# Kernel optimization log

Measured on AMD Instinct MI355X. Metric: run time of the kernel, lower is better.

The kernel has to match this reference:

```python
import jax, jax.numpy as jnp
import numpy as np

T, B, E, H = 2048, 4, 1024, 16
D = E // H  # head_dim = 64


def setup_inputs() -> dict:
    key = jax.random.key(0)
    k1, k2, k3, k4 = jax.random.split(key, 4)
    x = jax.random.normal(k1, (T, B, E), dtype=jnp.float32)
    # xavier-ish init scale
    Wqkv = jax.random.normal(k2, (3 * E, E), dtype=jnp.float32) * (1.0 / np.sqrt(2.0 * E))
    Wo = jax.random.normal(k3, (E, E), dtype=jnp.float32) * (1.0 / np.sqrt(E))
    key_padding_mask = jax.random.randint(k4, (B, T), 0, 2).astype(jnp.bool_)  # True = pad
    return {"x": x, "Wqkv": Wqkv, "Wo": Wo, "key_padding_mask": key_padding_mask}


def reference(x, Wqkv, Wo, key_padding_mask):
    t, b, e = x.shape
    h, d = H, E // H
    # fused QKV projection (bias=False)
    qkv = jnp.einsum('tbe,fe->tbf', x, Wqkv).reshape(t, b, 3, h, d)
    # chunk along the 3-axis, then permute to (B, H, T, D)
    q = jnp.transpose(qkv[:, :, 0], (1, 2, 0, 3))
    k = jnp.transpose(qkv[:, :, 1], (1, 2, 0, 3))
    v = jnp.transpose(qkv[:, :, 2], (1, 2, 0, 3))
    # SDPA with default scale 1/sqrt(head_dim); additive -inf mask on padded keys
    scale = 1.0 / jnp.sqrt(jnp.asarray(d, dtype=x.dtype))
    scores = jnp.einsum('bhtd,bhsd->bhts', q, k) * scale
    scores = jnp.where(key_padding_mask[:, None, None, :], -jnp.inf, scores)
    probs = jax.nn.softmax(scores, axis=-1)
    ctx = jnp.einsum('bhts,bhsd->bhtd', probs, v)  # (B,H,T,D)
    ctx = jnp.transpose(ctx, (0, 2, 1, 3)).reshape(b, t, e)  # (B,T,E)
    out = jnp.einsum('bte,fe->btf', ctx, Wo)  # out_proj, bias=False
    return jnp.transpose(out, (1, 0, 2))  # back to (T,B,E)
```

## Files before the change

kernel.cpp:

```cpp
#include <hip/hip_runtime.h>

typedef unsigned short u16;
typedef __bf16 bf16x8 __attribute__((ext_vector_type(8)));
typedef unsigned short u16x8 __attribute__((ext_vector_type(8)));
typedef unsigned short u16x4 __attribute__((ext_vector_type(4)));
typedef float f32x4 __attribute__((ext_vector_type(4)));

__device__ __forceinline__ f32x4 mfma16(u16x8 a, u16x8 b, f32x4 c) {
    return __builtin_amdgcn_mfma_f32_16x16x32_bf16(
        __builtin_bit_cast(bf16x8, a), __builtin_bit_cast(bf16x8, b), c, 0, 0, 0);
}

__device__ __forceinline__ u16 f2b(float f) {
    unsigned int u = __builtin_bit_cast(unsigned int, f);
    return (u16)((u + 0x7fffu + ((u >> 16) & 1u)) >> 16);
}

__device__ __forceinline__ f32x4 zero4() { f32x4 z = {0.f, 0.f, 0.f, 0.f}; return z; }

typedef __attribute__((address_space(1))) const unsigned int gas_u32;
typedef __attribute__((address_space(3))) unsigned int las_u32;
__device__ __forceinline__ void gload16(const u16* g, u16* l) {
    __builtin_amdgcn_global_load_lds((gas_u32*)g, (las_u32*)l, 16, 0, 0);
}

__device__ __forceinline__ u16x4 tr16(unsigned off) {
    u16x4 r;
    asm volatile("ds_read_b64_tr_b16 %0, %1" : "=v"(r) : "v"(off));
    return r;
}

__global__ __launch_bounds__(256) void cvt_bf16_kernel(const float* __restrict__ in,
                                                       u16* __restrict__ out, int n) {
    int i = (blockIdx.x * 256 + threadIdx.x) * 4;
    if (i >= n) return;
    float4 v = *reinterpret_cast<const float4*>(in + i);
    u16x4 o;
    o.x = f2b(v.x); o.y = f2b(v.y); o.z = f2b(v.z); o.w = f2b(v.w);
    *reinterpret_cast<u16x4*>(out + i) = o;
}

__global__ void detect_mask_kernel(const unsigned char* __restrict__ m, int* __restrict__ flag) {
    __shared__ int any;
    if (threadIdx.x == 0) any = 0;
    __syncthreads();
    int acc = 0;
    for (int i = threadIdx.x; i < 8192; i += 256)
        if (i & 3) acc |= m[i];
    if (acc) atomicOr(&any, 1);
    __syncthreads();
    if (threadIdx.x == 0) *flag = any ? 0 : 1;
}

template <int EPI>
__global__ __launch_bounds__(256)
void gemm_bt_kernel(const u16* __restrict__ A, const u16* __restrict__ Bt,
                    int M, int N, int K,
                    u16* __restrict__ qo, u16* __restrict__ ko, u16* __restrict__ vo,
                    float* __restrict__ fo) {
    constexpr int BK = 64;
    __shared__ __align__(16) u16 Al[128 * BK];
    __shared__ __align__(16) u16 Bl[128 * BK];
    int tid = threadIdx.x;
    int wave = tid >> 6, lane = tid & 63;
    int l15 = lane & 15, l16 = lane >> 4;
    int wr = wave >> 1, wc = wave & 1;
    int bx = blockIdx.x, by = blockIdx.y;

    const u16* gA[4]; const u16* gB[4]; u16* lA[4]; u16* lB[4];
#pragma unroll
    for (int q = 0; q < 4; q++) {
        int c = tid + q * 256;
        gA[q] = A + (size_t)(by * 128 + (c >> 3)) * K + (c & 7) * 8;
        gB[q] = Bt + (size_t)(bx * 128 + (c >> 3)) * K + (c & 7) * 8;
        lA[q] = Al + c * 8;
        lB[q] = Bl + c * 8;
    }

    f32x4 acc[4][4];
#pragma unroll
    for (int m = 0; m < 4; m++)
#pragma unroll
        for (int n = 0; n < 4; n++) acc[m][n] = zero4();

    for (int k0 = 0; k0 < K; k0 += BK) {
        __syncthreads();
#pragma unroll
        for (int q = 0; q < 4; q++) {
            gload16(gA[q] + k0, lA[q]);
            gload16(gB[q] + k0, lB[q]);
        }
        __syncthreads();
#pragma unroll
        for (int ks = 0; ks < 2; ks++) {
            u16x8 af[4], bfr[4];
#pragma unroll
            for (int m = 0; m < 4; m++)
                af[m] = *(const u16x8*)&Al[(wr * 64 + m * 16 + l15) * BK + ks * 32 + l16 * 8];
#pragma unroll
            for (int n = 0; n < 4; n++)
                bfr[n] = *(const u16x8*)&Bl[(wc * 64 + n * 16 + l15) * BK + ks * 32 + l16 * 8];
#pragma unroll
            for (int m = 0; m < 4; m++)
#pragma unroll
                for (int n = 0; n < 4; n++) acc[m][n] = mfma16(af[m], bfr[n], acc[m][n]);
        }
    }

#pragma unroll
    for (int m = 0; m < 4; m++) {
#pragma unroll
        for (int j = 0; j < 4; j++) {
            int row = by * 128 + wr * 64 + m * 16 + l16 * 4 + j;
#pragma unroll
            for (int n = 0; n < 4; n++) {
                int col = bx * 128 + wc * 64 + n * 16 + l15;
                float val = acc[m][n][j];
                if constexpr (EPI == 0) {
                    int chunk = col >> 10, h = (col >> 6) & 15, d = col & 63;
                    int t = row >> 2, bI = row & 3;
                    if (chunk == 0) val *= 0.18033688011112042f;
                    u16* dst = (chunk == 0) ? qo : (chunk == 1) ? ko : vo;
                    dst[((size_t)(bI * 16 + h) * 2048 + t) * 64 + d] = f2b(val);
                } else {
                    fo[(size_t)row * N + col] = val;
                }
            }
        }
    }
}

__global__ __launch_bounds__(256)
void attn_kernel(const u16* __restrict__ Qg, const u16* __restrict__ Kg,
                 const u16* __restrict__ Vg, const void* __restrict__ maskp,
                 const int* __restrict__ flag, u16* __restrict__ ctx) {
    __shared__ __align__(16) u16 Kl[32 * 72];
    __shared__ __align__(128) u16 Vs[2048];
    __shared__ __align__(16) u16 Pl[4][32 * 40];

    int tid = threadIdx.x;
    int wave = tid >> 6, lane = tid & 63;
    int l15 = lane & 15, l16 = lane >> 4;
    int bh = blockIdx.y;
    int b = bh >> 4, h = bh & 15;
    size_t base = (size_t)bh * 2048 * 64;
    int q0 = blockIdx.x * 128 + wave * 32;

    int isInt = *flag;
    const unsigned char* m8 = (const unsigned char*)maskp;
    const int* m32 = (const int*)maskp;

    u16x8 aq[2][2];
#pragma unroll
    for (int qb = 0; qb < 2; qb++)
#pragma unroll
        for (int ks = 0; ks < 2; ks++)
            aq[qb][ks] = *(const u16x8*)(Qg + base + (size_t)(q0 + qb * 16 + l15) * 64 +
                                         ks * 32 + l16 * 8);

    f32x4 acc_o[2][4];
    float mrun[2][4], plsum[2][4];
#pragma unroll
    for (int qb = 0; qb < 2; qb++) {
#pragma unroll
        for (int db = 0; db < 4; db++) acc_o[qb][db] = zero4();
#pragma unroll
        for (int j = 0; j < 4; j++) { mrun[qb][j] = -1e30f; plsum[qb][j] = 0.f; }
    }

    int srow = tid >> 3, schunk = tid & 7;
    const u16* kg = Kg + base + (size_t)srow * 64 + schunk * 8;
    const u16* vg = Vg + base + (size_t)srow * 64 + schunk * 8;
    u16* kldst = &Kl[srow * 72 + schunk * 8];
    u16* vsdst = &Vs[(schunk >> 1) * 512 + srow * 16 + (schunk & 1) * 8];
    unsigned vtrb = (unsigned)(uintptr_t)(&Vs[0]) + (unsigned)(l16 * 256 + l15 * 8);

    u16x8 kv = *(const u16x8*)kg;
    u16x8 vv = *(const u16x8*)vg;

    for (int it = 0; it < 64; ++it) {
        int s0 = it * 32;
        __syncthreads();
        *(u16x8*)kldst = kv;
        *(u16x8*)vsdst = vv;
        int snext = (s0 + 32) & 2047;
        u16x8 kv2 = *(const u16x8*)(kg + (size_t)snext * 64);
        u16x8 vv2 = *(const u16x8*)(vg + (size_t)snext * 64);
        __syncthreads();

        int ki = b * 2048 + s0 + l15;
        int pad0 = isInt ? (m32[ki] != 0) : (m8[ki] != 0);
        int pad1 = isInt ? (m32[ki + 16] != 0) : (m8[ki + 16] != 0);

        f32x4 sa[2][2];
        sa[0][0] = zero4(); sa[0][1] = zero4(); sa[1][0] = zero4(); sa[1][1] = zero4();
#pragma unroll
        for (int kb = 0; kb < 2; kb++)
#pragma unroll
            for (int ks = 0; ks < 2; ks++) {
                u16x8 bk = *(const u16x8*)&Kl[(kb * 16 + l15) * 72 + ks * 32 + l16 * 8];
                sa[0][kb] = mfma16(aq[0][ks], bk, sa[0][kb]);
                sa[1][kb] = mfma16(aq[1][ks], bk, sa[1][kb]);
            }

#pragma unroll
        for (int qb = 0; qb < 2; qb++) {
            float s0v[4], s1v[4];
            float gl = -1e30f;
#pragma unroll
            for (int j = 0; j < 4; j++) {
                s0v[j] = pad0 ? -1e30f : sa[qb][0][j];
                s1v[j] = pad1 ? -1e30f : sa[qb][1][j];
                gl = fmaxf(gl, fmaxf(s0v[j], s1v[j]) - mrun[qb][j]);
            }
            if (__any(gl > 8.0f)) {
                float tm[4];
#pragma unroll
                for (int j = 0; j < 4; j++) tm[j] = fmaxf(s0v[j], s1v[j]);
#pragma unroll
                for (int j = 0; j < 4; j++) {
                    tm[j] = fmaxf(tm[j], __shfl_xor(tm[j], 1));
                    tm[j] = fmaxf(tm[j], __shfl_xor(tm[j], 2));
                    tm[j] = fmaxf(tm[j], __shfl_xor(tm[j], 4));
                    tm[j] = fmaxf(tm[j], __shfl_xor(tm[j], 8));
                }
#pragma unroll
                for (int j = 0; j < 4; j++) {
                    float mnew = fmaxf(mrun[qb][j], tm[j]);
                    float sc = exp2f(mrun[qb][j] - mnew);
                    mrun[qb][j] = mnew;
                    plsum[qb][j] *= sc;
#pragma unroll
                    for (int db = 0; db < 4; db++) acc_o[qb][db][j] *= sc;
                }
            }
#pragma unroll
            for (int j = 0; j < 4; j++) {
                float p0 = exp2f(s0v[j] - mrun[qb][j]);
                float p1 = exp2f(s1v[j] - mrun[qb][j]);
                int prow = qb * 16 + l16 * 4 + j;
                Pl[wave][prow * 40 + l15] = f2b(p0);
                Pl[wave][prow * 40 + 16 + l15] = f2b(p1);
                plsum[qb][j] += p0 + p1;
            }
        }

        u16x8 ap0 = *(const u16x8*)&Pl[wave][(0 * 16 + l15) * 40 + l16 * 8];
        u16x8 ap1 = *(const u16x8*)&Pl[wave][(1 * 16 + l15) * 40 + l16 * 8];
#pragma unroll
        for (int db = 0; db < 4; db++) {
            u16x4 t0 = tr16(vtrb + db * 1024);
            u16x4 t1 = tr16(vtrb + db * 1024 + 128);
            asm volatile("s_waitcnt lgkmcnt(0)" ::: "memory");
            __builtin_amdgcn_sched_barrier(0);
            u16x8 bv = {t0[0], t0[1], t0[2], t0[3], t1[0], t1[1], t1[2], t1[3]};
            acc_o[0][db] = mfma16(ap0, bv, acc_o[0][db]);
            acc_o[1][db] = mfma16(ap1, bv, acc_o[1][db]);
        }
        kv = kv2; vv = vv2;
    }

#pragma unroll
    for (int qb = 0; qb < 2; qb++)
#pragma unroll
        for (int j = 0; j < 4; j++) {
            float rs = plsum[qb][j];
            rs += __shfl_xor(rs, 1);
            rs += __shfl_xor(rs, 2);
            rs += __shfl_xor(rs, 4);
            rs += __shfl_xor(rs, 8);
            float inv = 1.0f / rs;
            int qg = q0 + qb * 16 + l16 * 4 + j;
            size_t mrow = (size_t)qg * 4 + b;
#pragma unroll
            for (int db = 0; db < 4; db++)
                ctx[mrow * 1024 + h * 64 + db * 16 + l15] = f2b(acc_o[qb][db][j] * inv);
        }
}

extern "C" void kernel_launch(void* const* d_in, const int* in_sizes, int n_in,
                              void* d_out, int out_size, void* d_ws, size_t ws_size,
                              hipStream_t stream) {
    const float* x = (const float*)d_in[0];
    const float* wqkv = (const float*)d_in[1];
    const float* wo = (const float*)d_in[2];
    const void* mask = d_in[3];
    float* out = (float*)d_out;

    char* ws = (char*)d_ws;
    int* flag = (int*)ws;
    u16* xb = (u16*)(ws + 16);
    u16* wqkvb = xb + 8388608;
    u16* wob = wqkvb + 3145728;
    u16* qw = wob + 1048576;
    u16* kw = qw + 8388608;
    u16* vw = kw + 8388608;
    u16* ctx = xb;

    cvt_bf16_kernel<<<8192, 256, 0, stream>>>(x, xb, 8388608);
    cvt_bf16_kernel<<<3072, 256, 0, stream>>>(wqkv, wqkvb, 3145728);
    cvt_bf16_kernel<<<1024, 256, 0, stream>>>(wo, wob, 1048576);
    detect_mask_kernel<<<1, 256, 0, stream>>>((const unsigned char*)mask, flag);

    gemm_bt_kernel<0><<<dim3(24, 64), 256, 0, stream>>>(xb, wqkvb, 8192, 3072, 1024,
                                                        qw, kw, vw, nullptr);
    attn_kernel<<<dim3(16, 64), 256, 0, stream>>>(qw, kw, vw, mask, flag, ctx);
    gemm_bt_kernel<1><<<dim3(8, 64), 256, 0, stream>>>(ctx, wob, 8192, 1024, 1024,
                                                       nullptr, nullptr, nullptr, out);
}
```

Measured before the change: 451.9 us.

## Double attention key tile to 64 and batch V transposed loads before MFMAs

```diff
diff --git a/kernel.cpp b/kernel.cpp
--- a/kernel.cpp
+++ b/kernel.cpp
@@ -130,13 +130,13 @@
     }
 }
 
-__global__ __launch_bounds__(256)
+__global__ __launch_bounds__(256, 3)
 void attn_kernel(const u16* __restrict__ Qg, const u16* __restrict__ Kg,
                  const u16* __restrict__ Vg, const void* __restrict__ maskp,
                  const int* __restrict__ flag, u16* __restrict__ ctx) {
-    __shared__ __align__(16) u16 Kl[32 * 72];
-    __shared__ __align__(128) u16 Vs[2048];
-    __shared__ __align__(16) u16 Pl[4][32 * 40];
+    __shared__ __align__(16) u16 Kl[64 * 72];
+    __shared__ __align__(128) u16 Vs[4][64][16];
+    __shared__ __align__(16) u16 Pl[4][32 * 72];
 
     int tid = threadIdx.x;
     int wave = tid >> 6, lane = tid & 63;
@@ -168,55 +168,65 @@
         for (int j = 0; j < 4; j++) { mrun[qb][j] = -1e30f; plsum[qb][j] = 0.f; }
     }
 
-    int srow = tid >> 3, schunk = tid & 7;
-    const u16* kg = Kg + base + (size_t)srow * 64 + schunk * 8;
-    const u16* vg = Vg + base + (size_t)srow * 64 + schunk * 8;
-    u16* kldst = &Kl[srow * 72 + schunk * 8];
-    u16* vsdst = &Vs[(schunk >> 1) * 512 + srow * 16 + (schunk & 1) * 8];
-    unsigned vtrb = (unsigned)(uintptr_t)(&Vs[0]) + (unsigned)(l16 * 256 + l15 * 8);
-
-    u16x8 kv = *(const u16x8*)kg;
-    u16x8 vv = *(const u16x8*)vg;
-
-    for (int it = 0; it < 64; ++it) {
-        int s0 = it * 32;
+    int srow2 = tid >> 2, sc2 = tid & 3;
+    const u16* kg2 = Kg + base + (size_t)srow2 * 64 + sc2 * 16;
+    const u16* vg2 = Vg + base + (size_t)srow2 * 64 + sc2 * 16;
+    u16* kld = &Kl[srow2 * 72 + sc2 * 16];
+    u16* vsd = &Vs[sc2][srow2][0];
+    unsigned vtrb = (unsigned)(uintptr_t)(&Vs[0][0][0]) + (unsigned)(l16 * 256 + l15 * 8);
+
+    u16x8 ka = *(const u16x8*)kg2, kb_ = *(const u16x8*)(kg2 + 8);
+    u16x8 va = *(const u16x8*)vg2, vb_ = *(const u16x8*)(vg2 + 8);
+
+    for (int it = 0; it < 32; ++it) {
+        int s0 = it * 64;
         __syncthreads();
-        *(u16x8*)kldst = kv;
-        *(u16x8*)vsdst = vv;
-        int snext = (s0 + 32) & 2047;
-        u16x8 kv2 = *(const u16x8*)(kg + (size_t)snext * 64);
-        u16x8 vv2 = *(const u16x8*)(vg + (size_t)snext * 64);
+        *(u16x8*)kld = ka; *(u16x8*)(kld + 8) = kb_;
+        *(u16x8*)vsd = va; *(u16x8*)(vsd + 8) = vb_;
+        int snext = (s0 + 64) & 2047;
+        u16x8 kan = *(const u16x8*)(kg2 + (size_t)snext * 64);
+        u16x8 kbn = *(const u16x8*)(kg2 + (size_t)snext * 64 + 8);
+        u16x8 van = *(const u16x8*)(vg2 + (size_t)snext * 64);
+        u16x8 vbn = *(const u16x8*)(vg2 + (size_t)snext * 64 + 8);
         __syncthreads();
 
-        int ki = b * 2048 + s0 + l15;
-        int pad0 = isInt ? (m32[ki] != 0) : (m8[ki] != 0);
-        int pad1 = isInt ? (m32[ki + 16] != 0) : (m8[ki + 16] != 0);
-
-        f32x4 sa[2][2];
-        sa[0][0] = zero4(); sa[0][1] = zero4(); sa[1][0] = zero4(); sa[1][1] = zero4();
-#pragma unroll
-        for (int kb = 0; kb < 2; kb++)
+        int pad[4];
+#pragma unroll
+        for (int kb2 = 0; kb2 < 4; kb2++) {
+            int ki = b * 2048 + s0 + kb2 * 16 + l15;
+            pad[kb2] = isInt ? (m32[ki] != 0) : (m8[ki] != 0);
+        }
+
+        f32x4 sa[2][4];
+#pragma unroll
+        for (int kb2 = 0; kb2 < 4; kb2++) { sa[0][kb2] = zero4(); sa[1][kb2] = zero4(); }
+        __builtin_amdgcn_s_setprio(1);
+#pragma unroll
+        for (int kb2 = 0; kb2 < 4; kb2++)
 #pragma unroll
             for (int ks = 0; ks < 2; ks++) {
-                u16x8 bk = *(const u16x8*)&Kl[(kb * 16 + l15) * 72 + ks * 32 + l16 * 8];
-                sa[0][kb] = mfma16(aq[0][ks], bk, sa[0][kb]);
-                sa[1][kb] = mfma16(aq[1][ks], bk, sa[1][kb]);
-            }
+                u16x8 bk = *(const u16x8*)&Kl[(kb2 * 16 + l15) * 72 + ks * 32 + l16 * 8];
+                sa[0][kb2] = mfma16(aq[0][ks], bk, sa[0][kb2]);
+                sa[1][kb2] = mfma16(aq[1][ks], bk, sa[1][kb2]);
+            }
+        __builtin_amdgcn_s_setprio(0);
 
 #pragma unroll
         for (int qb = 0; qb < 2; qb++) {
-            float s0v[4], s1v[4];
+            float sv[4][4];
             float gl = -1e30f;
 #pragma unroll
-            for (int j = 0; j < 4; j++) {
-                s0v[j] = pad0 ? -1e30f : sa[qb][0][j];
-                s1v[j] = pad1 ? -1e30f : sa[qb][1][j];
-                gl = fmaxf(gl, fmaxf(s0v[j], s1v[j]) - mrun[qb][j]);
-            }
+            for (int kb2 = 0; kb2 < 4; kb2++)
+#pragma unroll
+                for (int j = 0; j < 4; j++) {
+                    sv[kb2][j] = pad[kb2] ? -1e30f : sa[qb][kb2][j];
+                    gl = fmaxf(gl, sv[kb2][j] - mrun[qb][j]);
+                }
             if (__any(gl > 8.0f)) {
                 float tm[4];
 #pragma unroll
-                for (int j = 0; j < 4; j++) tm[j] = fmaxf(s0v[j], s1v[j]);
+                for (int j = 0; j < 4; j++)
+                    tm[j] = fmaxf(fmaxf(sv[0][j], sv[1][j]), fmaxf(sv[2][j], sv[3][j]));
 #pragma unroll
                 for (int j = 0; j < 4; j++) {
                     tm[j] = fmaxf(tm[j], __shfl_xor(tm[j], 1));
@@ -236,28 +246,48 @@
             }
 #pragma unroll
             for (int j = 0; j < 4; j++) {
-                float p0 = exp2f(s0v[j] - mrun[qb][j]);
-                float p1 = exp2f(s1v[j] - mrun[qb][j]);
                 int prow = qb * 16 + l16 * 4 + j;
-                Pl[wave][prow * 40 + l15] = f2b(p0);
-                Pl[wave][prow * 40 + 16 + l15] = f2b(p1);
-                plsum[qb][j] += p0 + p1;
-            }
-        }
-
-        u16x8 ap0 = *(const u16x8*)&Pl[wave][(0 * 16 + l15) * 40 + l16 * 8];
-        u16x8 ap1 = *(const u16x8*)&Pl[wave][(1 * 16 + l15) * 40 + l16 * 8];
-#pragma unroll
-        for (int db = 0; db < 4; db++) {
-            u16x4 t0 = tr16(vtrb + db * 1024);
-            u16x4 t1 = tr16(vtrb + db * 1024 + 128);
-            asm volatile("s_waitcnt lgkmcnt(0)" ::: "memory");
-            __builtin_amdgcn_sched_barrier(0);
-            u16x8 bv = {t0[0], t0[1], t0[2], t0[3], t1[0], t1[1], t1[2], t1[3]};
-            acc_o[0][db] = mfma16(ap0, bv, acc_o[0][db]);
-            acc_o[1][db] = mfma16(ap1, bv, acc_o[1][db]);
-        }
-        kv = kv2; vv = vv2;
+                float ps = 0.f;
+#pragma unroll
+                for (int kb2 = 0; kb2 < 4; kb2++) {
+                    float p = exp2f(sv[kb2][j] - mrun[qb][j]);
+                    Pl[wave][prow * 72 + kb2 * 16 + l15] = f2b(p);
+                    ps += p;
+                }
+                plsum[qb][j] += ps;
+            }
+        }
+
+        u16x8 ap[2][2];
+#pragma unroll
+        for (int qb = 0; qb < 2; qb++)
+#pragma unroll
+            for (int ks2 = 0; ks2 < 2; ks2++)
+                ap[qb][ks2] = *(const u16x8*)&Pl[wave][(qb * 16 + l15) * 72 +
+                                                       ks2 * 32 + l16 * 8];
+        u16x4 t[4][2][2];
+#pragma unroll
+        for (int ks2 = 0; ks2 < 2; ks2++)
+#pragma unroll
+            for (int db = 0; db < 4; db++) {
+                t[db][ks2][0] = tr16(vtrb + db * 2048 + ks2 * 1024);
+                t[db][ks2][1] = tr16(vtrb + db * 2048 + ks2 * 1024 + 128);
+            }
+        asm volatile("s_waitcnt lgkmcnt(0)" ::: "memory");
+        __builtin_amdgcn_sched_barrier(0);
+        __builtin_amdgcn_s_setprio(1);
+#pragma unroll
+        for (int ks2 = 0; ks2 < 2; ks2++)
+#pragma unroll
+            for (int db = 0; db < 4; db++) {
+                u16x8 bv = {t[db][ks2][0][0], t[db][ks2][0][1], t[db][ks2][0][2],
+                            t[db][ks2][0][3], t[db][ks2][1][0], t[db][ks2][1][1],
+                            t[db][ks2][1][2], t[db][ks2][1][3]};
+                acc_o[0][db] = mfma16(ap[0][ks2], bv, acc_o[0][db]);
+                acc_o[1][db] = mfma16(ap[1][ks2], bv, acc_o[1][db]);
+            }
+        __builtin_amdgcn_s_setprio(0);
+        ka = kan; kb_ = kbn; va = van; vb_ = vbn;
     }
 
 #pragma unroll
```

Result: faster. 414.3 us (-8.3%).
